# Kernel optimization log

Hardware: AMD Instinct MI355X
Metric: run time of the kernel (lower is better)

The kernel has to match this reference:

```python
import jax, jax.numpy as jnp
import numpy as np

B, L, D, H, DEPTH, K = 16, 2048, 256, 8, 2, 7
HD = D // H
SCALE = HD ** -0.5


def _ln(x, g, b, eps=1e-5):
    m = x.mean(-1, keepdims=True)
    v = ((x - m) ** 2).mean(-1, keepdims=True)
    return (x - m) * jax.lax.rsqrt(v + eps) * g + b


def _nat_attn(x, qkv_w, qkv_b, proj_w, proj_b):
    # Neighborhood attention 1D: window of K tokens centered on each token,
    # clamped at sequence edges (NATTEN semantics, dilation=1).
    b, l, d = x.shape
    qkv = (x @ qkv_w + qkv_b).reshape(b, l, 3, H, HD).transpose(2, 0, 3, 1, 4)  # [3,B,H,L,hd]
    q, k, v = qkv[0] * SCALE, qkv[1], qkv[2]
    starts = jnp.clip(jnp.arange(l) - K // 2, 0, l - K)          # [L]
    idx = starts[:, None] + jnp.arange(K)                        # [L,K]
    kn = k[:, :, idx]                                            # [B,H,L,K,hd]
    vn = v[:, :, idx]
    attn = jax.nn.softmax(jnp.einsum('bhld,bhlkd->bhlk', q, kn), axis=-1)
    out = jnp.einsum('bhlk,bhlkd->bhld', attn, vn)               # [B,H,L,hd]
    out = out.transpose(0, 2, 1, 3).reshape(b, l, d)
    return out @ proj_w + proj_b


def _mlp(x, w1, b1, w2, b2):
    return jax.nn.gelu(x @ w1 + b1, approximate=False) @ w2 + b2


def setup_inputs() -> dict:
    key = jax.random.key(0)
    ks = jax.random.split(key, 8)
    s = 0.02
    return {
        'x': jax.random.normal(ks[0], (B, L, D), jnp.float32),
        'ln1_g': jnp.ones((DEPTH, D), jnp.float32),
        'ln1_b': jnp.zeros((DEPTH, D), jnp.float32),
        'qkv_w': jax.random.normal(ks[1], (DEPTH, D, 3 * D), jnp.float32) * s,
        'qkv_b': jnp.zeros((DEPTH, 3 * D), jnp.float32),
        'proj_w': jax.random.normal(ks[2], (DEPTH, D, D), jnp.float32) * s,
        'proj_b': jnp.zeros((DEPTH, D), jnp.float32),
        'ln2_g': jnp.ones((DEPTH, D), jnp.float32),
        'ln2_b': jnp.zeros((DEPTH, D), jnp.float32),
        'fc1_w': jax.random.normal(ks[3], (DEPTH, D, 4 * D), jnp.float32) * s,
        'fc1_b': jnp.zeros((DEPTH, 4 * D), jnp.float32),
        'fc2_w': jax.random.normal(ks[4], (DEPTH, 4 * D, D), jnp.float32) * s,
        'fc2_b': jnp.zeros((DEPTH, D), jnp.float32),
        'conv_w': jax.random.normal(ks[5], (2 * D, D, 3), jnp.float32) * s,  # OIH
        'dn_g': jnp.ones((2 * D,), jnp.float32),
        'dn_b': jnp.zeros((2 * D,), jnp.float32),
    }


def reference(x, ln1_g, ln1_b, qkv_w, qkv_b, proj_w, proj_b,
              ln2_g, ln2_b, fc1_w, fc1_b, fc2_w, fc2_b,
              conv_w, dn_g, dn_b):
    for i in range(DEPTH):
        h = _nat_attn(_ln(x, ln1_g[i], ln1_b[i]), qkv_w[i], qkv_b[i], proj_w[i], proj_b[i])
        x = x + h
        x = x + _mlp(_ln(x, ln2_g[i], ln2_b[i]), fc1_w[i], fc1_b[i], fc2_w[i], fc2_b[i])
    # ConvDownsampler: Conv1d(D, 2D, k=3, s=2, p=1, bias=False) + LayerNorm
    xc = x.transpose(0, 2, 1)  # [B,C,L]
    y = jax.lax.conv_general_dilated(xc, conv_w, window_strides=(2,),
                                     padding=[(1, 1)],
                                     dimension_numbers=('NCH', 'OIH', 'NCH'))
    y = y.transpose(0, 2, 1)   # [B, L//2, 2D]
    y = _ln(y, dn_g, dn_b)
    return (y, x)
```

## Files before the change

kernel.cpp:

```cpp
#include <hip/hip_runtime.h>

typedef unsigned short u16;
typedef __attribute__((ext_vector_type(8))) short bf16x8;
typedef __attribute__((ext_vector_type(4))) float f32x4;

__device__ __forceinline__ float bf2f(u16 u) { return __uint_as_float(((unsigned)u) << 16); }
__device__ __forceinline__ u16 f2bf(float f) {
    unsigned u = __float_as_uint(f);
    return (u16)((u + 0x7FFFu + ((u >> 16) & 1u)) >> 16);
}

__device__ __forceinline__ float gelu_fast(float v) {
    float u = v * (1.5957691216057308f + 0.07135481282700722f * v * v);
    return v * (1.f / (1.f + __expf(-u)));
}

__device__ __forceinline__ void load_lds16(const u16* g, u16* l) {
    __builtin_amdgcn_global_load_lds(
        (const __attribute__((address_space(1))) unsigned int*)g,
        (__attribute__((address_space(3))) unsigned int*)l,
        16, 0, 0);
}

template<int EPI>
__global__ __launch_bounds__(256) void gemm_kernel(
    const u16* __restrict__ A, const u16* __restrict__ Wt,
    const float* __restrict__ bias, const float* __restrict__ res,
    void* __restrict__ outp, int M, int N, int K)
{
    __shared__ __align__(16) u16 As[128 * 64];
    __shared__ __align__(16) u16 Bs[128 * 64];
    const int tid  = threadIdx.x;
    const int lane = tid & 63;
    const int wave = tid >> 6;
    const int row0 = blockIdx.x * 128;
    const int col0 = blockIdx.y * 128;
    const int wr = (wave >> 1) * 64;
    const int wc = (wave & 1) * 64;
    const int lr = lane & 15;
    const int q  = lane >> 4;

    f32x4 acc[4][4];
#pragma unroll
    for (int i = 0; i < 4; ++i)
#pragma unroll
        for (int j = 0; j < 4; ++j) acc[i][j] = (f32x4){0.f, 0.f, 0.f, 0.f};

    const int strow  = tid >> 3;
    const int schunk = (tid & 7) ^ (strow & 7);
    const u16* ag = A  + (size_t)(row0 + strow) * K + schunk * 8;
    const u16* bg = Wt + (size_t)(col0 + strow) * K + schunk * 8;
    const size_t rstep32 = (size_t)32 * K;
    u16* alp = As + tid * 8;
    u16* blp = Bs + tid * 8;

    for (int k0 = 0; k0 < K; k0 += 64) {
        __syncthreads();
#pragma unroll
        for (int s = 0; s < 4; ++s) {
            load_lds16(ag + s * rstep32 + k0, alp + s * 2048);
            load_lds16(bg + s * rstep32 + k0, blp + s * 2048);
        }
        __syncthreads();
#pragma unroll
        for (int kk = 0; kk < 2; ++kk) {
            bf16x8 af[4], bfv[4];
#pragma unroll
            for (int i = 0; i < 4; ++i) {
                const int r = wr + i * 16 + lr;
                af[i] = *(const bf16x8*)(As + r * 64 + (((kk * 4 + q) ^ (r & 7)) * 8));
            }
#pragma unroll
            for (int j = 0; j < 4; ++j) {
                const int r = wc + j * 16 + lr;
                bfv[j] = *(const bf16x8*)(Bs + r * 64 + (((kk * 4 + q) ^ (r & 7)) * 8));
            }
#pragma unroll
            for (int i = 0; i < 4; ++i)
#pragma unroll
                for (int j = 0; j < 4; ++j)
                    acc[i][j] = __builtin_amdgcn_mfma_f32_16x16x32_bf16(bfv[j], af[i], acc[i][j], 0, 0, 0);
        }
    }

#pragma unroll
    for (int j = 0; j < 4; ++j) {
        const int cb = col0 + wc + j * 16 + q * 4;
        float4 bv;
        if (EPI == 3) { bv.x = bv.y = bv.z = bv.w = 0.f; }
        else          { bv = *(const float4*)(bias + cb); }
#pragma unroll
        for (int i = 0; i < 4; ++i) {
            const int row = row0 + wr + i * 16 + lr;
            float v0 = acc[i][j][0] + bv.x;
            float v1 = acc[i][j][1] + bv.y;
            float v2 = acc[i][j][2] + bv.z;
            float v3 = acc[i][j][3] + bv.w;
            if (EPI == 1) {
                const size_t o = (size_t)row * N + cb;
                const float4 rr = *(const float4*)(res + o);
                float4 ov;
                ov.x = v0 + rr.x; ov.y = v1 + rr.y; ov.z = v2 + rr.z; ov.w = v3 + rr.w;
                *(float4*)((float*)outp + o) = ov;
            } else {
                if (EPI == 2) {
                    v0 = gelu_fast(v0); v1 = gelu_fast(v1);
                    v2 = gelu_fast(v2); v3 = gelu_fast(v3);
                }
                ushort4 ov;
                ov.x = f2bf(v0); ov.y = f2bf(v1); ov.z = f2bf(v2); ov.w = f2bf(v3);
                *(ushort4*)((u16*)outp + (size_t)row * N + cb) = ov;
            }
        }
    }
}

__global__ __launch_bounds__(256) void ln_f2b_kernel(
    const float* __restrict__ x, const float* __restrict__ g,
    const float* __restrict__ be, u16* __restrict__ out)
{
    const int lane = threadIdx.x & 63;
    const int row  = blockIdx.x * 4 + (threadIdx.x >> 6);
    const float4 a = *(const float4*)(x + (size_t)row * 256 + lane * 4);
    float v[4] = {a.x, a.y, a.z, a.w};
    float s = v[0] + v[1] + v[2] + v[3];
#pragma unroll
    for (int m = 1; m < 64; m <<= 1) s += __shfl_xor(s, m);
    const float mean = s * (1.f / 256.f);
    float s2 = 0.f;
#pragma unroll
    for (int e = 0; e < 4; ++e) { float d = v[e] - mean; s2 += d * d; }
#pragma unroll
    for (int m = 1; m < 64; m <<= 1) s2 += __shfl_xor(s2, m);
    const float rstd = rsqrtf(s2 * (1.f / 256.f) + 1e-5f);
    const float4 gg = *(const float4*)(g + lane * 4);
    const float4 bb = *(const float4*)(be + lane * 4);
    ushort4 o;
    o.x = f2bf((v[0] - mean) * rstd * gg.x + bb.x);
    o.y = f2bf((v[1] - mean) * rstd * gg.y + bb.y);
    o.z = f2bf((v[2] - mean) * rstd * gg.z + bb.z);
    o.w = f2bf((v[3] - mean) * rstd * gg.w + bb.w);
    *(ushort4*)(out + (size_t)row * 256 + lane * 4) = o;
}

__global__ __launch_bounds__(256) void ln_b2f_kernel(
    const u16* __restrict__ x, const float* __restrict__ g,
    const float* __restrict__ be, float* __restrict__ out)
{
    const int lane = threadIdx.x & 63;
    const int row  = blockIdx.x * 4 + (threadIdx.x >> 6);
    const u16* xr = x + (size_t)row * 512 + lane * 8;
    float v[8];
#pragma unroll
    for (int e = 0; e < 8; e += 4) {
        ushort4 a = *(const ushort4*)(xr + e);
        v[e] = bf2f(a.x); v[e+1] = bf2f(a.y); v[e+2] = bf2f(a.z); v[e+3] = bf2f(a.w);
    }
    float s = 0.f;
#pragma unroll
    for (int e = 0; e < 8; ++e) s += v[e];
#pragma unroll
    for (int m = 1; m < 64; m <<= 1) s += __shfl_xor(s, m);
    const float mean = s * (1.f / 512.f);
    float s2 = 0.f;
#pragma unroll
    for (int e = 0; e < 8; ++e) { float d = v[e] - mean; s2 += d * d; }
#pragma unroll
    for (int m = 1; m < 64; m <<= 1) s2 += __shfl_xor(s2, m);
    const float rstd = rsqrtf(s2 * (1.f / 512.f) + 1e-5f);
    float* orow = out + (size_t)row * 512 + lane * 8;
#pragma unroll
    for (int e = 0; e < 8; e += 4) {
        float4 o;
        o.x = (v[e]   - mean) * rstd * g[lane*8+e]   + be[lane*8+e];
        o.y = (v[e+1] - mean) * rstd * g[lane*8+e+1] + be[lane*8+e+1];
        o.z = (v[e+2] - mean) * rstd * g[lane*8+e+2] + be[lane*8+e+2];
        o.w = (v[e+3] - mean) * rstd * g[lane*8+e+3] + be[lane*8+e+3];
        *(float4*)(orow + e) = o;
    }
}

__global__ __launch_bounds__(256) void attn_kernel(
    const u16* __restrict__ qkv, u16* __restrict__ out)
{
    const int lane  = threadIdx.x & 63;
    const int token = blockIdx.x * 4 + (threadIdx.x >> 6);
    const int b = token >> 11;
    const int l = token & 2047;
    const int h = lane >> 3;
    const int s = lane & 7;
    const int off = h * 32 + s * 4;

    ushort4 q4 = *(const ushort4*)(qkv + (size_t)token * 768 + off);
    const float scale = 0.17677669529663687f;
    float q0 = bf2f(q4.x), q1 = bf2f(q4.y), q2 = bf2f(q4.z), q3 = bf2f(q4.w);

    int start = l - 3;
    start = start < 0 ? 0 : (start > 2041 ? 2041 : start);
    const u16* kbase = qkv + ((size_t)(b << 11) + start) * 768 + 256 + off;

    float sc[7], vv[7][4];
#pragma unroll
    for (int j = 0; j < 7; ++j) {
        const u16* kp = kbase + (size_t)j * 768;
        ushort4 k4 = *(const ushort4*)kp;
        ushort4 v4 = *(const ushort4*)(kp + 256);
        float d = q0 * bf2f(k4.x) + q1 * bf2f(k4.y) + q2 * bf2f(k4.z) + q3 * bf2f(k4.w);
        d += __shfl_xor(d, 1); d += __shfl_xor(d, 2); d += __shfl_xor(d, 4);
        sc[j] = d * scale;
        vv[j][0] = bf2f(v4.x); vv[j][1] = bf2f(v4.y); vv[j][2] = bf2f(v4.z); vv[j][3] = bf2f(v4.w);
    }
    float mx = sc[0];
#pragma unroll
    for (int j = 1; j < 7; ++j) mx = fmaxf(mx, sc[j]);
    float p[7], sum = 0.f;
#pragma unroll
    for (int j = 0; j < 7; ++j) { p[j] = __expf(sc[j] - mx); sum += p[j]; }
    const float inv = 1.f / sum;
    float o0 = 0, o1 = 0, o2 = 0, o3 = 0;
#pragma unroll
    for (int j = 0; j < 7; ++j) {
        o0 += p[j] * vv[j][0]; o1 += p[j] * vv[j][1];
        o2 += p[j] * vv[j][2]; o3 += p[j] * vv[j][3];
    }
    ushort4 o;
    o.x = f2bf(o0 * inv); o.y = f2bf(o1 * inv); o.z = f2bf(o2 * inv); o.w = f2bf(o3 * inv);
    *(ushort4*)(out + (size_t)token * 256 + off) = o;
}

__global__ __launch_bounds__(256) void transpose_kernel(
    const float* __restrict__ in, u16* __restrict__ out, int K, int N)
{
    __shared__ float t[32][33];
    const int n0 = blockIdx.x * 32;
    const int k0 = blockIdx.y * 32;
    const int d  = blockIdx.z;
    const int tr = threadIdx.x >> 3;
    const int tc = (threadIdx.x & 7) * 4;
    const float4 a = *(const float4*)(in + ((size_t)d * K + k0 + tr) * N + n0 + tc);
    t[tc + 0][tr] = a.x; t[tc + 1][tr] = a.y; t[tc + 2][tr] = a.z; t[tc + 3][tr] = a.w;
    __syncthreads();
    ushort4 o;
    o.x = f2bf(t[tr][tc + 0]); o.y = f2bf(t[tr][tc + 1]);
    o.z = f2bf(t[tr][tc + 2]); o.w = f2bf(t[tr][tc + 3]);
    *(ushort4*)(out + ((size_t)d * N + n0 + tr) * K + k0 + tc) = o;
}

__global__ void convw_kernel(const float* __restrict__ in, u16* __restrict__ out)
{
    int idx = blockIdx.x * 256 + threadIdx.x;
    int r  = idx % 768;
    int co = idx / 768;
    int t  = r / 256;
    int ci = r % 256;
    out[idx] = f2bf(in[(size_t)co * 768 + (size_t)ci * 3 + t]);
}

__global__ __launch_bounds__(256) void im2col_kernel(
    const float* __restrict__ x, u16* __restrict__ x2, int r0)
{
    int idx = blockIdx.x * 256 + threadIdx.x;
    int c4  = idx & 63;
    int t   = (idx >> 6) % 3;
    int rl  = idx / 192;
    int row = r0 + rl;
    int b   = row >> 10;
    int lo  = row & 1023;
    int l   = 2 * lo + t - 1;
    ushort4 o = {0, 0, 0, 0};
    if (l >= 0 && l < 2048) {
        float4 val = *(const float4*)(x + ((size_t)(b << 11) + l) * 256 + c4 * 4);
        o.x = f2bf(val.x); o.y = f2bf(val.y); o.z = f2bf(val.z); o.w = f2bf(val.w);
    }
    *(ushort4*)(x2 + (size_t)rl * 768 + t * 256 + c4 * 4) = o;
}

extern "C" void kernel_launch(void* const* d_in, const int* in_sizes, int n_in,
                              void* d_out, int out_size, void* d_ws, size_t ws_size,
                              hipStream_t stream)
{
    const float* x_in   = (const float*)d_in[0];
    const float* ln1_g  = (const float*)d_in[1];
    const float* ln1_b  = (const float*)d_in[2];
    const float* qkv_w  = (const float*)d_in[3];
    const float* qkv_b  = (const float*)d_in[4];
    const float* proj_w = (const float*)d_in[5];
    const float* proj_b = (const float*)d_in[6];
    const float* ln2_g  = (const float*)d_in[7];
    const float* ln2_b  = (const float*)d_in[8];
    const float* fc1_w  = (const float*)d_in[9];
    const float* fc1_b  = (const float*)d_in[10];
    const float* fc2_w  = (const float*)d_in[11];
    const float* fc2_b  = (const float*)d_in[12];
    const float* conv_w = (const float*)d_in[13];
    const float* dn_g   = (const float*)d_in[14];
    const float* dn_b   = (const float*)d_in[15];

    float* xbuf = (float*)d_out + 8388608;
    u16*   xn   = (u16*)d_out;

    char* ws = (char*)d_ws;
    const size_t MB = 1024ull * 1024;
    u16* qkv_wt  = (u16*)ws;
    u16* proj_wt = qkv_wt  + 2 * 768 * 256;
    u16* fc1_wt  = proj_wt + 2 * 256 * 256;
    u16* fc2_wt  = fc1_wt  + 2 * 1024 * 256;
    u16* conv_wt = fc2_wt  + 2 * 256 * 1024;
    u16* S       = (u16*)(ws + 4 * MB);

    const size_t R = ws_size > 4 * MB ? ws_size - 4 * MB : 0;
    int nb = 16;    while (nb > 1 && (size_t)nb * 4 * MB > R) nb >>= 1;
    int Mf = 32768; while (Mf > 2048 && (size_t)Mf * 2048 > R) Mf >>= 1;
    int Mc = 16384; while (Mc > 2048 && (size_t)Mc * 2560 > R) Mc >>= 1;

    transpose_kernel<<<dim3(768 / 32, 256 / 32, 2), 256, 0, stream>>>(qkv_w,  qkv_wt,  256, 768);
    transpose_kernel<<<dim3(256 / 32, 256 / 32, 2), 256, 0, stream>>>(proj_w, proj_wt, 256, 256);
    transpose_kernel<<<dim3(1024 / 32, 256 / 32, 2), 256, 0, stream>>>(fc1_w, fc1_wt, 256, 1024);
    transpose_kernel<<<dim3(256 / 32, 1024 / 32, 2), 256, 0, stream>>>(fc2_w, fc2_wt, 1024, 256);
    convw_kernel<<<(512 * 768) / 256, 256, 0, stream>>>(conv_w, conv_wt);

    for (int layer = 0; layer < 2; ++layer) {
        const float* l1g = ln1_g + layer * 256;
        const float* l1b = ln1_b + layer * 256;
        const float* l2g = ln2_g + layer * 256;
        const float* l2b = ln2_b + layer * 256;
        const u16*   qwt = qkv_wt  + (size_t)layer * 768 * 256;
        const float* qb  = qkv_b   + layer * 768;
        const u16*   pwt = proj_wt + (size_t)layer * 256 * 256;
        const float* pb  = proj_b  + layer * 256;
        const u16*   f1w = fc1_wt  + (size_t)layer * 1024 * 256;
        const float* f1b = fc1_b   + layer * 1024;
        const u16*   f2w = fc2_wt  + (size_t)layer * 256 * 1024;
        const float* f2b = fc2_b   + layer * 256;

        const float* xsrc = (layer == 0) ? x_in : xbuf;

        ln_f2b_kernel<<<8192, 256, 0, stream>>>(xsrc, l1g, l1b, xn);
        {
            const int Mg = nb * 2048;
            u16* qkvc  = S;
            u16* atnoc = S + (size_t)Mg * 768;
            for (int g = 0; g < 16 / nb; ++g) {
                const size_t t0 = (size_t)g * Mg;
                gemm_kernel<0><<<dim3(Mg / 128, 6), 256, 0, stream>>>(
                    xn + t0 * 256, qwt, qb, nullptr, qkvc, Mg, 768, 256);
                attn_kernel<<<Mg / 4, 256, 0, stream>>>(qkvc, atnoc);
                gemm_kernel<1><<<dim3(Mg / 128, 2), 256, 0, stream>>>(
                    atnoc, pwt, pb, xsrc + t0 * 256, xbuf + t0 * 256, Mg, 256, 256);
            }
        }
        ln_f2b_kernel<<<8192, 256, 0, stream>>>(xbuf, l2g, l2b, xn);
        {
            u16* hbuf = S;
            for (int qq = 0; qq < 32768 / Mf; ++qq) {
                const size_t r0 = (size_t)qq * Mf;
                gemm_kernel<2><<<dim3(Mf / 128, 8), 256, 0, stream>>>(
                    xn + r0 * 256, f1w, f1b, nullptr, hbuf, Mf, 1024, 256);
                gemm_kernel<1><<<dim3(Mf / 128, 2), 256, 0, stream>>>(
                    hbuf, f2w, f2b, xbuf + r0 * 256, xbuf + r0 * 256, Mf, 256, 1024);
            }
        }
    }

    {
        u16* x2c = S;
        u16* ycc = S + (size_t)Mc * 768;
        for (int c = 0; c < 16384 / Mc; ++c) {
            const int r0 = c * Mc;
            im2col_kernel<<<3 * Mc / 4, 256, 0, stream>>>(xbuf, x2c, r0);
            gemm_kernel<3><<<dim3(Mc / 128, 4), 256, 0, stream>>>(
                x2c, conv_wt, nullptr, nullptr, ycc, Mc, 512, 768);
            ln_b2f_kernel<<<Mc / 4, 256, 0, stream>>>(
                ycc, dn_g, dn_b, (float*)d_out + (size_t)r0 * 512);
        }
    }
}
```

Before: 508.3 us.

## Fuse MLP fc1+GELU+fc2 into one kernel keeping hidden activations in LDS

Replaces the two-GEMM MLP (fc1 with GELU epilogue writing a bf16 hidden buffer, then fc2 with residual) with a single kernel that processes 128 rows per block. It loads the normalized input tile to LDS, computes the hidden dimension in 128-wide chunks with GELU, stores each chunk to LDS and accumulates into fc2 immediately. This removes the global round trip of the 32768x1024 hidden tensor. In exchange, weights are read directly from global/L2 per wave without LDS staging, and only 256 blocks are launched, which limits parallelism.

```diff
diff --git a/kernel.cpp b/kernel.cpp
--- a/kernel.cpp
+++ b/kernel.cpp
@@ -103,14 +103,124 @@
                 ov.x = v0 + rr.x; ov.y = v1 + rr.y; ov.z = v2 + rr.z; ov.w = v3 + rr.w;
                 *(float4*)((float*)outp + o) = ov;
             } else {
-                if (EPI == 2) {
-                    v0 = gelu_fast(v0); v1 = gelu_fast(v1);
-                    v2 = gelu_fast(v2); v3 = gelu_fast(v3);
-                }
                 ushort4 ov;
                 ov.x = f2bf(v0); ov.y = f2bf(v1); ov.z = f2bf(v2); ov.w = f2bf(v3);
                 *(ushort4*)((u16*)outp + (size_t)row * N + cb) = ov;
             }
+        }
+    }
+}
+
+__global__ __launch_bounds__(512, 2) void fused_mlp_kernel(
+    const u16* __restrict__ xn, const u16* __restrict__ W1t,
+    const float* __restrict__ b1, const u16* __restrict__ W2t,
+    const float* __restrict__ b2, const float* __restrict__ res,
+    float* __restrict__ out)
+{
+    __shared__ __align__(16) u16 As[128 * 256];
+    __shared__ __align__(16) u16 Hs[128 * 128];
+    const int tid  = threadIdx.x;
+    const int lane = tid & 63;
+    const int wave = tid >> 6;
+    const int r0   = blockIdx.x * 128;
+    const int wr   = (wave >> 2) * 64;
+    const int wq   = wave & 3;
+    const int lr   = lane & 15;
+    const int q    = lane >> 4;
+
+#pragma unroll
+    for (int s = 0; s < 8; ++s) {
+        const int idx = s * 512 + tid;
+        const int row = idx >> 5;
+        const int ch  = (idx & 31) ^ (row & 7);
+        load_lds16(xn + (size_t)(r0 + row) * 256 + ch * 8, As + idx * 8);
+    }
+
+    f32x4 acc2[4][4];
+#pragma unroll
+    for (int i = 0; i < 4; ++i)
+#pragma unroll
+        for (int j = 0; j < 4; ++j) acc2[i][j] = (f32x4){0.f, 0.f, 0.f, 0.f};
+
+    __syncthreads();
+
+    for (int c = 0; c < 8; ++c) {
+        f32x4 acc1[4][2];
+#pragma unroll
+        for (int i = 0; i < 4; ++i)
+#pragma unroll
+            for (int j = 0; j < 2; ++j) acc1[i][j] = (f32x4){0.f, 0.f, 0.f, 0.f};
+        const u16* w1c = W1t + (size_t)(c * 128 + wq * 32) * 256;
+#pragma unroll
+        for (int kk = 0; kk < 8; ++kk) {
+            bf16x8 wf[2], af[4];
+#pragma unroll
+            for (int j = 0; j < 2; ++j)
+                wf[j] = *(const bf16x8*)(w1c + (size_t)(j * 16 + lr) * 256 + kk * 32 + q * 8);
+#pragma unroll
+            for (int i = 0; i < 4; ++i) {
+                const int r = wr + i * 16 + lr;
+                af[i] = *(const bf16x8*)(As + r * 256 + (((kk * 4 + q) ^ (r & 7)) * 8));
+            }
+#pragma unroll
+            for (int i = 0; i < 4; ++i)
+#pragma unroll
+                for (int j = 0; j < 2; ++j)
+                    acc1[i][j] = __builtin_amdgcn_mfma_f32_16x16x32_bf16(wf[j], af[i], acc1[i][j], 0, 0, 0);
+        }
+        __syncthreads();
+#pragma unroll
+        for (int j = 0; j < 2; ++j) {
+            const int coln = wq * 32 + j * 16 + q * 4;
+            const float4 bb = *(const float4*)(b1 + c * 128 + coln);
+#pragma unroll
+            for (int i = 0; i < 4; ++i) {
+                const int row = wr + i * 16 + lr;
+                ushort4 hh;
+                hh.x = f2bf(gelu_fast(acc1[i][j][0] + bb.x));
+                hh.y = f2bf(gelu_fast(acc1[i][j][1] + bb.y));
+                hh.z = f2bf(gelu_fast(acc1[i][j][2] + bb.z));
+                hh.w = f2bf(gelu_fast(acc1[i][j][3] + bb.w));
+                const int slot = (coln >> 3) ^ (row & 7);
+                *(ushort4*)(Hs + row * 128 + slot * 8 + (q & 1) * 4) = hh;
+            }
+        }
+        __syncthreads();
+        const u16* w2c = W2t + (size_t)(wq * 64) * 1024 + c * 128;
+#pragma unroll
+        for (int kk = 0; kk < 4; ++kk) {
+            bf16x8 wf2[4], ah[4];
+#pragma unroll
+            for (int j = 0; j < 4; ++j)
+                wf2[j] = *(const bf16x8*)(w2c + (size_t)(j * 16 + lr) * 1024 + kk * 32 + q * 8);
+#pragma unroll
+            for (int i = 0; i < 4; ++i) {
+                const int r = wr + i * 16 + lr;
+                ah[i] = *(const bf16x8*)(Hs + r * 128 + (((kk * 4 + q) ^ (r & 7)) * 8));
+            }
+#pragma unroll
+            for (int i = 0; i < 4; ++i)
+#pragma unroll
+                for (int j = 0; j < 4; ++j)
+                    acc2[i][j] = __builtin_amdgcn_mfma_f32_16x16x32_bf16(wf2[j], ah[i], acc2[i][j], 0, 0, 0);
+        }
+    }
+
+#pragma unroll
+    for (int j = 0; j < 4; ++j) {
+        const int col = wq * 64 + j * 16 + q * 4;
+        const float4 bb = *(const float4*)(b2 + col);
+#pragma unroll
+        for (int i = 0; i < 4; ++i) {
+            const int row = r0 + wr + i * 16 + lr;
+            const size_t o = (size_t)row * 256 + col;
+            const float4 rr = *(const float4*)(res + o);
+            float4 ov;
+            ov.x = acc2[i][j][0] + bb.x + rr.x;
+            ov.y = acc2[i][j][1] + bb.y + rr.y;
+            ov.z = acc2[i][j][2] + bb.z + rr.z;
+            ov.w = acc2[i][j][3] + bb.w + rr.w;
+            *(float4*)(out + o) = ov;
         }
     }
 }
@@ -310,7 +420,6 @@
 
     const size_t R = ws_size > 4 * MB ? ws_size - 4 * MB : 0;
     int nb = 16;    while (nb > 1 && (size_t)nb * 4 * MB > R) nb >>= 1;
-    int Mf = 32768; while (Mf > 2048 && (size_t)Mf * 2048 > R) Mf >>= 1;
     int Mc = 16384; while (Mc > 2048 && (size_t)Mc * 2560 > R) Mc >>= 1;
 
     transpose_kernel<<<dim3(768 / 32, 256 / 32, 2), 256, 0, stream>>>(qkv_w,  qkv_wt,  256, 768);
@@ -350,16 +459,7 @@
             }
         }
         ln_f2b_kernel<<<8192, 256, 0, stream>>>(xbuf, l2g, l2b, xn);
-        {
-            u16* hbuf = S;
-            for (int qq = 0; qq < 32768 / Mf; ++qq) {
-                const size_t r0 = (size_t)qq * Mf;
-                gemm_kernel<2><<<dim3(Mf / 128, 8), 256, 0, stream>>>(
-                    xn + r0 * 256, f1w, f1b, nullptr, hbuf, Mf, 1024, 256);
-                gemm_kernel<1><<<dim3(Mf / 128, 2), 256, 0, stream>>>(
-                    hbuf, f2w, f2b, xbuf + r0 * 256, xbuf + r0 * 256, Mf, 256, 1024);
-            }
-        }
+        fused_mlp_kernel<<<256, 512, 0, stream>>>(xn, f1w, f1b, f2w, f2b, xbuf, xbuf);
     }
 
     {
```

Result: slower. 527.0 us (+3.7%).

## Double-buffer GEMM LDS tiles with K=32 steps to overlap loads and MFMA

Applied to the files above, without the earlier changes.

The GEMM main loop now uses two LDS buffers of 128x32 per operand and prefetches the next K-slice via global_load_lds while the current slice feeds the MFMAs. This removes one of the two barriers per iteration and lets memory latency overlap with compute. The price is halving the K-step, so there are twice as many iterations and barriers, plus a new swizzle pattern. The epilogue is also reordered to hoist the bias loads.

```diff
diff --git a/kernel.cpp b/kernel.cpp
--- a/kernel.cpp
+++ b/kernel.cpp
@@ -28,8 +28,8 @@
     const float* __restrict__ bias, const float* __restrict__ res,
     void* __restrict__ outp, int M, int N, int K)
 {
-    __shared__ __align__(16) u16 As[128 * 64];
-    __shared__ __align__(16) u16 Bs[128 * 64];
+    __shared__ __align__(16) u16 As[2][128 * 32];
+    __shared__ __align__(16) u16 Bs[2][128 * 32];
     const int tid  = threadIdx.x;
     const int lane = tid & 63;
     const int wave = tid >> 6;
@@ -46,56 +46,69 @@
 #pragma unroll
         for (int j = 0; j < 4; ++j) acc[i][j] = (f32x4){0.f, 0.f, 0.f, 0.f};
 
-    const int strow  = tid >> 3;
-    const int schunk = (tid & 7) ^ (strow & 7);
-    const u16* ag = A  + (size_t)(row0 + strow) * K + schunk * 8;
-    const u16* bg = Wt + (size_t)(col0 + strow) * K + schunk * 8;
-    const size_t rstep32 = (size_t)32 * K;
-    u16* alp = As + tid * 8;
-    u16* blp = Bs + tid * 8;
-
-    for (int k0 = 0; k0 < K; k0 += 64) {
+    const int u0 = tid, u1 = tid + 256;
+    const int r_u0 = u0 >> 2, r_u1 = u1 >> 2;
+    const int c_u0 = (u0 & 3) ^ ((u0 >> 3) & 3);
+    const int c_u1 = (u1 & 3) ^ ((u1 >> 3) & 3);
+    const u16* agA0 = A  + (size_t)(row0 + r_u0) * K + c_u0 * 8;
+    const u16* agA1 = A  + (size_t)(row0 + r_u1) * K + c_u1 * 8;
+    const u16* bgB0 = Wt + (size_t)(col0 + r_u0) * K + c_u0 * 8;
+    const u16* bgB1 = Wt + (size_t)(col0 + r_u1) * K + c_u1 * 8;
+
+    const int nt = K >> 5;
+
+    load_lds16(agA0, As[0] + u0 * 8);
+    load_lds16(agA1, As[0] + u1 * 8);
+    load_lds16(bgB0, Bs[0] + u0 * 8);
+    load_lds16(bgB1, Bs[0] + u1 * 8);
+    __syncthreads();
+
+    for (int t = 0; t < nt; ++t) {
+        if (t + 1 < nt) {
+            const int p = (t + 1) & 1;
+            const int k0 = (t + 1) << 5;
+            load_lds16(agA0 + k0, As[p] + u0 * 8);
+            load_lds16(agA1 + k0, As[p] + u1 * 8);
+            load_lds16(bgB0 + k0, Bs[p] + u0 * 8);
+            load_lds16(bgB1 + k0, Bs[p] + u1 * 8);
+        }
+        const u16* Ab = As[t & 1];
+        const u16* Bb = Bs[t & 1];
+        bf16x8 af[4], bfv[4];
+#pragma unroll
+        for (int i = 0; i < 4; ++i) {
+            const int r = wr + i * 16 + lr;
+            af[i] = *(const bf16x8*)(Ab + r * 32 + ((q ^ ((r >> 1) & 3)) * 8));
+        }
+#pragma unroll
+        for (int j = 0; j < 4; ++j) {
+            const int r = wc + j * 16 + lr;
+            bfv[j] = *(const bf16x8*)(Bb + r * 32 + ((q ^ ((r >> 1) & 3)) * 8));
+        }
+#pragma unroll
+        for (int i = 0; i < 4; ++i)
+#pragma unroll
+            for (int j = 0; j < 4; ++j)
+                acc[i][j] = __builtin_amdgcn_mfma_f32_16x16x32_bf16(bfv[j], af[i], acc[i][j], 0, 0, 0);
         __syncthreads();
-#pragma unroll
-        for (int s = 0; s < 4; ++s) {
-            load_lds16(ag + s * rstep32 + k0, alp + s * 2048);
-            load_lds16(bg + s * rstep32 + k0, blp + s * 2048);
-        }
-        __syncthreads();
-#pragma unroll
-        for (int kk = 0; kk < 2; ++kk) {
-            bf16x8 af[4], bfv[4];
-#pragma unroll
-            for (int i = 0; i < 4; ++i) {
-                const int r = wr + i * 16 + lr;
-                af[i] = *(const bf16x8*)(As + r * 64 + (((kk * 4 + q) ^ (r & 7)) * 8));
-            }
-#pragma unroll
-            for (int j = 0; j < 4; ++j) {
-                const int r = wc + j * 16 + lr;
-                bfv[j] = *(const bf16x8*)(Bs + r * 64 + (((kk * 4 + q) ^ (r & 7)) * 8));
-            }
-#pragma unroll
-            for (int i = 0; i < 4; ++i)
-#pragma unroll
-                for (int j = 0; j < 4; ++j)
-                    acc[i][j] = __builtin_amdgcn_mfma_f32_16x16x32_bf16(bfv[j], af[i], acc[i][j], 0, 0, 0);
-        }
-    }
-
+    }
+
+    float4 bv[4];
 #pragma unroll
     for (int j = 0; j < 4; ++j) {
-        const int cb = col0 + wc + j * 16 + q * 4;
-        float4 bv;
-        if (EPI == 3) { bv.x = bv.y = bv.z = bv.w = 0.f; }
-        else          { bv = *(const float4*)(bias + cb); }
-#pragma unroll
-        for (int i = 0; i < 4; ++i) {
-            const int row = row0 + wr + i * 16 + lr;
-            float v0 = acc[i][j][0] + bv.x;
-            float v1 = acc[i][j][1] + bv.y;
-            float v2 = acc[i][j][2] + bv.z;
-            float v3 = acc[i][j][3] + bv.w;
+        if (EPI == 3) { bv[j].x = bv[j].y = bv[j].z = bv[j].w = 0.f; }
+        else          { bv[j] = *(const float4*)(bias + col0 + wc + j * 16 + q * 4); }
+    }
+#pragma unroll
+    for (int i = 0; i < 4; ++i) {
+        const int row = row0 + wr + i * 16 + lr;
+#pragma unroll
+        for (int j = 0; j < 4; ++j) {
+            const int cb = col0 + wc + j * 16 + q * 4;
+            float v0 = acc[i][j][0] + bv[j].x;
+            float v1 = acc[i][j][1] + bv[j].y;
+            float v2 = acc[i][j][2] + bv[j].z;
+            float v3 = acc[i][j][3] + bv[j].w;
             if (EPI == 1) {
                 const size_t o = (size_t)row * N + cb;
                 const float4 rr = *(const float4*)(res + o);
```

Result: no change. 501.9 us (-1.3%).

## Restructure GEMM to stage full-K activation tiles in LDS and stream weights from global

Applied to the files above, without the earlier changes.

Replaces the 128x128 LDS-tiled GEMM with a kernel that stages a 64-row by 256-K activation slab in LDS, double-buffered across K chunks, while each wave reads its weight fragments straight from global/L2 into registers. Each block covers several 128-column tiles (NT), which cuts how often the A tile is reloaded and the number of barriers per K step. Occupancy is raised with launch_bounds(256,2). The cost is uncoalesced, latency-exposed weight loads that rely on L2 hits, plus more accumulator registers for the wider tiles.

```diff
diff --git a/kernel.cpp b/kernel.cpp
--- a/kernel.cpp
+++ b/kernel.cpp
@@ -22,94 +22,104 @@
         16, 0, 0);
 }
 
-template<int EPI>
-__global__ __launch_bounds__(256) void gemm_kernel(
+template<int EPI, int NT, int NKC>
+__global__ __launch_bounds__(256, 2) void gemm_nk(
     const u16* __restrict__ A, const u16* __restrict__ Wt,
     const float* __restrict__ bias, const float* __restrict__ res,
-    void* __restrict__ outp, int M, int N, int K)
-{
-    __shared__ __align__(16) u16 As[128 * 64];
-    __shared__ __align__(16) u16 Bs[128 * 64];
+    void* __restrict__ outp, int N)
+{
+    __shared__ __align__(16) u16 As[(NKC > 1) ? 2 : 1][64 * 256];
     const int tid  = threadIdx.x;
     const int lane = tid & 63;
-    const int wave = tid >> 6;
-    const int row0 = blockIdx.x * 128;
-    const int col0 = blockIdx.y * 128;
-    const int wr = (wave >> 1) * 64;
-    const int wc = (wave & 1) * 64;
-    const int lr = lane & 15;
-    const int q  = lane >> 4;
-
-    f32x4 acc[4][4];
-#pragma unroll
-    for (int i = 0; i < 4; ++i)
-#pragma unroll
-        for (int j = 0; j < 4; ++j) acc[i][j] = (f32x4){0.f, 0.f, 0.f, 0.f};
-
-    const int strow  = tid >> 3;
-    const int schunk = (tid & 7) ^ (strow & 7);
-    const u16* ag = A  + (size_t)(row0 + strow) * K + schunk * 8;
-    const u16* bg = Wt + (size_t)(col0 + strow) * K + schunk * 8;
-    const size_t rstep32 = (size_t)32 * K;
-    u16* alp = As + tid * 8;
-    u16* blp = Bs + tid * 8;
-
-    for (int k0 = 0; k0 < K; k0 += 64) {
-        __syncthreads();
-#pragma unroll
-        for (int s = 0; s < 4; ++s) {
-            load_lds16(ag + s * rstep32 + k0, alp + s * 2048);
-            load_lds16(bg + s * rstep32 + k0, blp + s * 2048);
-        }
-        __syncthreads();
-#pragma unroll
-        for (int kk = 0; kk < 2; ++kk) {
-            bf16x8 af[4], bfv[4];
+    const int wq   = tid >> 6;
+    const int r0   = blockIdx.x * 64;
+    const int c0   = blockIdx.y * (NT * 128);
+    const int lr   = lane & 15;
+    const int q    = lane >> 4;
+    const int K    = NKC * 256;
+
+    f32x4 acc[NT][4][2];
+#pragma unroll
+    for (int t = 0; t < NT; ++t)
+#pragma unroll
+        for (int i = 0; i < 4; ++i)
+#pragma unroll
+            for (int j = 0; j < 2; ++j) acc[t][i][j] = (f32x4){0.f, 0.f, 0.f, 0.f};
+
+    const int strow  = tid >> 5;
+    const int schunk = (tid & 31) ^ (strow & 7);
+    const u16* ag = A + (size_t)(r0 + strow) * K + schunk * 8;
+
+    auto stage = [&](int buf, int kc) {
+        const u16* src = ag + kc * 256;
+        u16* dst = (u16*)As[buf] + tid * 8;
+#pragma unroll
+        for (int s = 0; s < 8; ++s)
+            load_lds16(src + (size_t)s * 8 * K, dst + s * 2048);
+    };
+
+    stage(0, 0);
+    __syncthreads();
+
+    const u16* wbase = Wt + (size_t)(c0 + wq * 32 + lr) * K + q * 8;
+
+#pragma unroll 1
+    for (int kc = 0; kc < NKC; ++kc) {
+        if (NKC > 1 && kc + 1 < NKC) stage((kc + 1) & 1, kc + 1);
+        const u16* Ab = As[(NKC > 1) ? (kc & 1) : 0];
+#pragma unroll
+        for (int kk = 0; kk < 8; ++kk) {
+            bf16x8 af[4];
 #pragma unroll
             for (int i = 0; i < 4; ++i) {
-                const int r = wr + i * 16 + lr;
-                af[i] = *(const bf16x8*)(As + r * 64 + (((kk * 4 + q) ^ (r & 7)) * 8));
-            }
-#pragma unroll
-            for (int j = 0; j < 4; ++j) {
-                const int r = wc + j * 16 + lr;
-                bfv[j] = *(const bf16x8*)(Bs + r * 64 + (((kk * 4 + q) ^ (r & 7)) * 8));
-            }
-#pragma unroll
-            for (int i = 0; i < 4; ++i)
-#pragma unroll
-                for (int j = 0; j < 4; ++j)
-                    acc[i][j] = __builtin_amdgcn_mfma_f32_16x16x32_bf16(bfv[j], af[i], acc[i][j], 0, 0, 0);
-        }
-    }
-
-#pragma unroll
-    for (int j = 0; j < 4; ++j) {
-        const int cb = col0 + wc + j * 16 + q * 4;
-        float4 bv;
-        if (EPI == 3) { bv.x = bv.y = bv.z = bv.w = 0.f; }
-        else          { bv = *(const float4*)(bias + cb); }
-#pragma unroll
-        for (int i = 0; i < 4; ++i) {
-            const int row = row0 + wr + i * 16 + lr;
-            float v0 = acc[i][j][0] + bv.x;
-            float v1 = acc[i][j][1] + bv.y;
-            float v2 = acc[i][j][2] + bv.z;
-            float v3 = acc[i][j][3] + bv.w;
-            if (EPI == 1) {
-                const size_t o = (size_t)row * N + cb;
-                const float4 rr = *(const float4*)(res + o);
-                float4 ov;
-                ov.x = v0 + rr.x; ov.y = v1 + rr.y; ov.z = v2 + rr.z; ov.w = v3 + rr.w;
-                *(float4*)((float*)outp + o) = ov;
-            } else {
-                if (EPI == 2) {
-                    v0 = gelu_fast(v0); v1 = gelu_fast(v1);
-                    v2 = gelu_fast(v2); v3 = gelu_fast(v3);
+                const int r = i * 16 + lr;
+                af[i] = *(const bf16x8*)(Ab + r * 256 + (((kk * 4 + q) ^ (r & 7)) * 8));
+            }
+#pragma unroll
+            for (int t = 0; t < NT; ++t) {
+                const u16* wp = wbase + (size_t)(t * 128) * K + kc * 256 + kk * 32;
+                const bf16x8 wf0 = *(const bf16x8*)(wp);
+                const bf16x8 wf1 = *(const bf16x8*)(wp + (size_t)16 * K);
+#pragma unroll
+                for (int i = 0; i < 4; ++i) {
+                    acc[t][i][0] = __builtin_amdgcn_mfma_f32_16x16x32_bf16(wf0, af[i], acc[t][i][0], 0, 0, 0);
+                    acc[t][i][1] = __builtin_amdgcn_mfma_f32_16x16x32_bf16(wf1, af[i], acc[t][i][1], 0, 0, 0);
                 }
-                ushort4 ov;
-                ov.x = f2bf(v0); ov.y = f2bf(v1); ov.z = f2bf(v2); ov.w = f2bf(v3);
-                *(ushort4*)((u16*)outp + (size_t)row * N + cb) = ov;
+            }
+        }
+        if (NKC > 1 && kc + 1 < NKC) __syncthreads();
+    }
+
+#pragma unroll
+    for (int t = 0; t < NT; ++t) {
+#pragma unroll
+        for (int j = 0; j < 2; ++j) {
+            const int cb = c0 + t * 128 + wq * 32 + j * 16 + q * 4;
+            float4 bv;
+            if (EPI == 3) { bv.x = bv.y = bv.z = bv.w = 0.f; }
+            else          { bv = *(const float4*)(bias + cb); }
+#pragma unroll
+            for (int i = 0; i < 4; ++i) {
+                const int row = r0 + i * 16 + lr;
+                float v0 = acc[t][i][j][0] + bv.x;
+                float v1 = acc[t][i][j][1] + bv.y;
+                float v2 = acc[t][i][j][2] + bv.z;
+                float v3 = acc[t][i][j][3] + bv.w;
+                if (EPI == 1) {
+                    const size_t o = (size_t)row * N + cb;
+                    const float4 rr = *(const float4*)(res + o);
+                    float4 ov;
+                    ov.x = v0 + rr.x; ov.y = v1 + rr.y; ov.z = v2 + rr.z; ov.w = v3 + rr.w;
+                    *(float4*)((float*)outp + o) = ov;
+                } else {
+                    if (EPI == 2) {
+                        v0 = gelu_fast(v0); v1 = gelu_fast(v1);
+                        v2 = gelu_fast(v2); v3 = gelu_fast(v3);
+                    }
+                    ushort4 ov;
+                    ov.x = f2bf(v0); ov.y = f2bf(v1); ov.z = f2bf(v2); ov.w = f2bf(v3);
+                    *(ushort4*)((u16*)outp + (size_t)row * N + cb) = ov;
+                }
             }
         }
     }
@@ -342,11 +352,11 @@
             u16* atnoc = S + (size_t)Mg * 768;
             for (int g = 0; g < 16 / nb; ++g) {
                 const size_t t0 = (size_t)g * Mg;
-                gemm_kernel<0><<<dim3(Mg / 128, 6), 256, 0, stream>>>(
-                    xn + t0 * 256, qwt, qb, nullptr, qkvc, Mg, 768, 256);
+                gemm_nk<0, 3, 1><<<dim3(Mg / 64, 2), 256, 0, stream>>>(
+                    xn + t0 * 256, qwt, qb, nullptr, qkvc, 768);
                 attn_kernel<<<Mg / 4, 256, 0, stream>>>(qkvc, atnoc);
-                gemm_kernel<1><<<dim3(Mg / 128, 2), 256, 0, stream>>>(
-                    atnoc, pwt, pb, xsrc + t0 * 256, xbuf + t0 * 256, Mg, 256, 256);
+                gemm_nk<1, 2, 1><<<dim3(Mg / 64, 1), 256, 0, stream>>>(
+                    atnoc, pwt, pb, xsrc + t0 * 256, xbuf + t0 * 256, 256);
             }
         }
         ln_f2b_kernel<<<8192, 256, 0, stream>>>(xbuf, l2g, l2b, xn);
@@ -354,10 +364,10 @@
             u16* hbuf = S;
             for (int qq = 0; qq < 32768 / Mf; ++qq) {
                 const size_t r0 = (size_t)qq * Mf;
-                gemm_kernel<2><<<dim3(Mf / 128, 8), 256, 0, stream>>>(
-                    xn + r0 * 256, f1w, f1b, nullptr, hbuf, Mf, 1024, 256);
-                gemm_kernel<1><<<dim3(Mf / 128, 2), 256, 0, stream>>>(
-                    hbuf, f2w, f2b, xbuf + r0 * 256, xbuf + r0 * 256, Mf, 256, 1024);
+                gemm_nk<2, 4, 1><<<dim3(Mf / 64, 2), 256, 0, stream>>>(
+                    xn + r0 * 256, f1w, f1b, nullptr, hbuf, 1024);
+                gemm_nk<1, 2, 4><<<dim3(Mf / 64, 1), 256, 0, stream>>>(
+                    hbuf, f2w, f2b, xbuf + r0 * 256, xbuf + r0 * 256, 256);
             }
         }
     }
@@ -368,8 +378,8 @@
         for (int c = 0; c < 16384 / Mc; ++c) {
             const int r0 = c * Mc;
             im2col_kernel<<<3 * Mc / 4, 256, 0, stream>>>(xbuf, x2c, r0);
-            gemm_kernel<3><<<dim3(Mc / 128, 4), 256, 0, stream>>>(
-                x2c, conv_wt, nullptr, nullptr, ycc, Mc, 512, 768);
+            gemm_nk<3, 2, 3><<<dim3(Mc / 64, 2), 256, 0, stream>>>(
+                x2c, conv_wt, nullptr, nullptr, ycc, 512);
             ln_b2f_kernel<<<Mc / 4, 256, 0, stream>>>(
                 ycc, dn_g, dn_b, (float*)d_out + (size_t)r0 * 512);
         }
```

Measured after the change: 579.4 us. 14.0% more time.
